# Kernel optimization log

Hardware: AMD Instinct MI355X
Metric: run time of the kernel (lower is better)

Reference implementation:

```python
import jax, jax.numpy as jnp
import numpy as np

B, S, F, D, NH, K, NB = 128, 200, 32, 512, 4, 4, 2
Dh = D // NH
UP = 704  # round(1.3*512) up to multiple of 64
FD = 7    # forecast_days
EPS = 1e-5


def _layernorm(x, w):
    mu = x.mean(-1, keepdims=True)
    var = ((x - mu) ** 2).mean(-1, keepdims=True)
    return (x - mu) / jnp.sqrt(var + EPS) * w


def _forward(x, w_in, b_in, ln1_w, conv_w, conv_b, w_gates, r_gates, b_gates,
             gn_w, ln2_w, ff_up, ff_down, post_ln_w, fc1_w, fc1_b, fc2_w, fc2_b):
    b, s, _ = x.shape
    h = x @ w_in + b_in  # (B,S,D) input projection
    for blk in range(NB):
        xn = _layernorm(h, ln1_w[blk])
        # causal depthwise conv1d (kernel K) + swish, feeds i/f gates
        xp = jnp.pad(xn, ((0, 0), (K - 1, 0), (0, 0)))
        xc = conv_b[blk] + sum(conv_w[blk, k] * xp[:, k:k + s, :] for k in range(K))
        xc = xc * jax.nn.sigmoid(xc)  # swish
        xch = xc.reshape(b, s, NH, Dh)
        xnh = xn.reshape(b, s, NH, Dh)
        # headwise (block-diagonal) gate projections
        ipre = jnp.einsum('bshd,hde->bshe', xch, w_gates[blk, 0])
        fpre = jnp.einsum('bshd,hde->bshe', xch, w_gates[blk, 1])
        zpre = jnp.einsum('bshd,hde->bshe', xnh, w_gates[blk, 2])
        opre = jnp.einsum('bshd,hde->bshe', xnh, w_gates[blk, 3])
        pre = jnp.stack([ipre, fpre, zpre, opre], 0)        # (4,B,S,NH,Dh)
        pre = jnp.transpose(pre, (2, 0, 1, 3, 4))           # (S,4,B,NH,Dh)
        R = r_gates[blk]                                     # (4,NH,Dh,Dh)
        bg = b_gates[blk].reshape(4, NH, Dh)

        def step(carry, g):
            hs, cs, ns, ms = carry  # each (B,NH,Dh)
            rec = jnp.einsum('bhd,ghde->gbhe', hs, R)
            iraw = g[0] + rec[0] + bg[0]
            fraw = g[1] + rec[1] + bg[1]
            zraw = g[2] + rec[2] + bg[2]
            oraw = g[3] + rec[3] + bg[3]
            # stabilized exponential gating (vanilla sLSTM backend)
            logf = ms + jax.nn.log_sigmoid(fraw)
            m_new = jnp.maximum(iraw, logf)
            ig = jnp.exp(iraw - m_new)
            fg = jnp.exp(logf - m_new)
            c_new = fg * cs + ig * jnp.tanh(zraw)
            n_new = fg * ns + ig
            h_new = jax.nn.sigmoid(oraw) * c_new / n_new
            return (h_new, c_new, n_new, m_new), h_new

        z0 = jnp.zeros((b, NH, Dh), x.dtype)
        _, hseq = jax.lax.scan(step, (z0, z0, z0, z0), pre)  # (S,B,NH,Dh)
        # multi-head groupnorm (per head, over Dh)
        mu = hseq.mean(-1, keepdims=True)
        var = ((hseq - mu) ** 2).mean(-1, keepdims=True)
        y = (hseq - mu) / jnp.sqrt(var + EPS) * gn_w[blk].reshape(NH, Dh)
        y = jnp.transpose(y, (1, 0, 2, 3)).reshape(b, s, D)
        h = h + y  # residual
        # gated GeLU feedforward with residual
        xn2 = _layernorm(h, ln2_w[blk])
        u = xn2 @ ff_up[blk]                                 # (B,S,2*UP)
        gate, up = jnp.split(u, 2, -1)
        h = h + (jax.nn.gelu(gate) * up) @ ff_down[blk]
    h = _layernorm(h, post_ln_w)  # post-blocks norm
    last = h[:, -1, :]
    out = jax.nn.relu(last @ fc1_w + fc1_b) @ fc2_w + fc2_b  # (B,FD)
    return out


def setup_inputs() -> dict:
    key = jax.random.key(0)
    ks = jax.random.split(key, 12)

    def rn(k, shape, s=0.02):
        return jax.random.normal(k, shape, jnp.float32) * s

    return {
        'x': jax.random.normal(ks[0], (B, S, F), jnp.float32),
        'w_in': rn(ks[1], (F, D), 0.1),
        'b_in': jnp.zeros((D,), jnp.float32),
        'ln1_w': jnp.ones((NB, D), jnp.float32),
        'conv_w': rn(ks[2], (NB, K, D), 0.1),
        'conv_b': jnp.zeros((NB, D), jnp.float32),
        'w_gates': rn(ks[3], (NB, 4, NH, Dh, Dh), 0.05),
        'r_gates': rn(ks[4], (NB, 4, NH, Dh, Dh), 0.05),
        'b_gates': rn(ks[5], (NB, 4, D), 0.1),
        'gn_w': jnp.ones((NB, D), jnp.float32),
        'ln2_w': jnp.ones((NB, D), jnp.float32),
        'ff_up': rn(ks[6], (NB, D, 2 * UP), 0.05),
        'ff_down': rn(ks[7], (NB, UP, D), 0.05),
        'post_ln_w': jnp.ones((D,), jnp.float32),
        'fc1_w': rn(ks[8], (D, D // 2), 0.05),
        'fc1_b': jnp.zeros((D // 2,), jnp.float32),
        'fc2_w': rn(ks[9], (D // 2, FD), 0.05),
        'fc2_b': jnp.zeros((FD,), jnp.float32),
    }


def reference(x, w_in, b_in, ln1_w, conv_w, conv_b, w_gates, r_gates, b_gates,
              gn_w, ln2_w, ff_up, ff_down, post_ln_w, fc1_w, fc1_b, fc2_w, fc2_b):
    return _forward(x, w_in, b_in, ln1_w, conv_w, conv_b, w_gates, r_gates, b_gates,
                    gn_w, ln2_w, ff_up, ff_down, post_ln_w, fc1_w, fc1_b, fc2_w, fc2_b)
```

## Files before the change

### kernel.cpp

```cpp
#include <hip/hip_runtime.h>

#define B_  128
#define S_  200
#define F_  32
#define D_  512
#define NH_ 4
#define DH_ 128
#define KK_ 4
#define NB_ 2
#define UP_ 704
#define FD_ 7
#define M_  (B_*S_)

typedef unsigned short u16;
typedef _Float16 f16;
typedef __attribute__((ext_vector_type(8))) _Float16 f16x8;
typedef __attribute__((ext_vector_type(8))) short  s16x8;
typedef __attribute__((ext_vector_type(4))) float  f32x4;

__device__ __forceinline__ u16 f2bf(float f){
  unsigned x = __builtin_bit_cast(unsigned, f);
  return (u16)((x + 0x7fffu + ((x>>16)&1u)) >> 16);
}
__device__ __forceinline__ float bf2f(u16 u){
  return __builtin_bit_cast(float, (unsigned)u << 16);
}
__device__ __forceinline__ f32x4 mfma16(s16x8 a, s16x8 b, f32x4 c){
  return __builtin_amdgcn_mfma_f32_16x16x32_bf16(a, b, c, 0, 0, 0);
}
__device__ __forceinline__ f32x4 mfma16h(f16x8 a, f16x8 b, f32x4 c){
  return __builtin_amdgcn_mfma_f32_16x16x32_f16(a, b, c, 0, 0, 0);
}
__device__ __forceinline__ float frcp(float x){ return __builtin_amdgcn_rcpf(x); }
__device__ __forceinline__ float tanh_fast(float z){
  const float u = __expf(-2.f*fabsf(z));
  const float t = (1.f-u)*frcp(1.f+u);
  return copysignf(t, z);
}
__device__ __forceinline__ float logsig_fast(float f){
  const float t = __expf(-fabsf(f));
  return fminf(f, 0.f) - __logf(1.f + t);
}
__device__ __forceinline__ float sigmoid_fast(float x){
  return frcp(1.f + __expf(-x));
}
__device__ __forceinline__ void bar_lgkm(){
  __builtin_amdgcn_sched_barrier(0);
  asm volatile("s_waitcnt lgkmcnt(0)" ::: "memory");
  __builtin_amdgcn_s_barrier();
  __builtin_amdgcn_sched_barrier(0);
}
template<int CTRL>
__device__ __forceinline__ float dpp_add(float v){
  int x = __builtin_amdgcn_update_dpp(0, __builtin_bit_cast(int, v), CTRL, 0xf, 0xf, false);
  return v + __builtin_bit_cast(float, x);
}
__device__ __forceinline__ float wave_sum64(float v){
  v = dpp_add<0x111>(v);
  v = dpp_add<0x112>(v);
  v = dpp_add<0x114>(v);
  v = dpp_add<0x118>(v);
  v = dpp_add<0x142>(v);
  v = dpp_add<0x143>(v);
  return __builtin_bit_cast(float, __builtin_amdgcn_readlane(__builtin_bit_cast(int, v), 63));
}

__global__ void k_cast(const float* __restrict__ in, u16* __restrict__ out, int n){
  int i = blockIdx.x*256 + threadIdx.x;
  if (i < n) out[i] = f2bf(in[i]);
}
__global__ void k_cast_up(const float* __restrict__ in, u16* __restrict__ out, int n){
  int i = blockIdx.x*256 + threadIdx.x;
  if (i >= n) return;
  const int np   = i % (2*UP_);
  const int rest = i / (2*UP_);
  const int k = np >> 7, j = np & 127;
  const int col = (j < 64) ? (k*64 + j) : (UP_ + k*64 + (j - 64));
  out[i] = f2bf(in[(size_t)rest*(2*UP_) + col]);
}
__global__ void k_zero(float* __restrict__ p, int n){
  int i = blockIdx.x*256 + threadIdx.x;
  if (i < n) p[i] = 0.f;
}
__global__ void k_sentinel(float* __restrict__ out, int n){
  int i = blockIdx.x*256 + threadIdx.x;
  if (i < n) out[i] = -12345.0f;
}

__global__ __launch_bounds__(256) void k_inproj(const float* __restrict__ x,
    const float* __restrict__ w, const float* __restrict__ bias, float* __restrict__ h)
{
  __shared__ float xs[8][32];
  const int m0 = blockIdx.x*8, tid = threadIdx.x;
  xs[tid>>5][tid&31] = x[(size_t)(m0 + (tid>>5))*F_ + (tid&31)];
  __syncthreads();
  #pragma unroll
  for (int hf=0; hf<2; ++hf){
    const int e = tid + hf*256;
    float a[8];
    const float bb = bias[e];
    #pragma unroll
    for (int r=0;r<8;r++) a[r]=bb;
    for (int f=0; f<F_; ++f){
      const float wv = w[(size_t)f*D_ + e];
      #pragma unroll
      for (int r=0;r<8;r++) a[r] += xs[r][f]*wv;
    }
    #pragma unroll
    for (int r=0;r<8;r++) h[(size_t)(m0+r)*D_ + e] = a[r];
  }
}

__global__ __launch_bounds__(128) void k_ln(const float* __restrict__ in, const float* __restrict__ w,
      u16* __restrict__ outb)
{
  const int row = blockIdx.x, tid = threadIdx.x;
  const f32x4* rp = (const f32x4*)(in + (size_t)row*D_);
  f32x4 v = rp[tid];
  float s = v[0]+v[1]+v[2]+v[3];
  float q = v[0]*v[0]+v[1]*v[1]+v[2]*v[2]+v[3]*v[3];
  #pragma unroll
  for (int off=32; off; off>>=1){ s += __shfl_down(s,off,64); q += __shfl_down(q,off,64); }
  __shared__ float red[2][2];
  if ((tid&63)==0){ red[tid>>6][0]=s; red[tid>>6][1]=q; }
  __syncthreads();
  const float sum = red[0][0]+red[1][0], sq = red[0][1]+red[1][1];
  const float mu  = sum*(1.f/D_);
  const float var = sq*(1.f/D_) - mu*mu;
  const float inv = rsqrtf(var + 1e-5f);
  f32x4 wv = ((const f32x4*)w)[tid];
  ushort4 ob;
  ob.x=f2bf((v[0]-mu)*inv*wv[0]); ob.y=f2bf((v[1]-mu)*inv*wv[1]);
  ob.z=f2bf((v[2]-mu)*inv*wv[2]); ob.w=f2bf((v[3]-mu)*inv*wv[3]);
  ((ushort4*)(outb + (size_t)row*D_))[tid] = ob;
}

__global__ __launch_bounds__(128) void k_addln(float* __restrict__ h, const u16* __restrict__ y,
      const float* __restrict__ w, u16* __restrict__ outb)
{
  const int row = blockIdx.x, tid = threadIdx.x;
  f32x4 v = ((const f32x4*)(h + (size_t)row*D_))[tid];
  ushort4 yq = ((const ushort4*)(y + (size_t)row*D_))[tid];
  v[0]+=bf2f(yq.x); v[1]+=bf2f(yq.y); v[2]+=bf2f(yq.z); v[3]+=bf2f(yq.w);
  ((f32x4*)(h + (size_t)row*D_))[tid] = v;
  float s = v[0]+v[1]+v[2]+v[3];
  float q = v[0]*v[0]+v[1]*v[1]+v[2]*v[2]+v[3]*v[3];
  #pragma unroll
  for (int off=32; off; off>>=1){ s += __shfl_down(s,off,64); q += __shfl_down(q,off,64); }
  __shared__ float red[2][2];
  if ((tid&63)==0){ red[tid>>6][0]=s; red[tid>>6][1]=q; }
  __syncthreads();
  const float sum = red[0][0]+red[1][0], sq = red[0][1]+red[1][1];
  const float mu  = sum*(1.f/D_);
  const float var = sq*(1.f/D_) - mu*mu;
  const float inv = rsqrtf(var + 1e-5f);
  f32x4 wv = ((const f32x4*)w)[tid];
  ushort4 ob;
  ob.x=f2bf((v[0]-mu)*inv*wv[0]); ob.y=f2bf((v[1]-mu)*inv*wv[1]);
  ob.z=f2bf((v[2]-mu)*inv*wv[2]); ob.w=f2bf((v[3]-mu)*inv*wv[3]);
  ((ushort4*)(outb + (size_t)row*D_))[tid] = ob;
}

__global__ void k_conv(const u16* __restrict__ xnbf, const float* __restrict__ cw,
                       const float* __restrict__ cb, u16* __restrict__ xcc,
                       int s0, int Sc)
{
  const int idx = blockIdx.x*256 + threadIdx.x;
  const int e4 = idx & 127;
  const int sl = (idx >> 7) % Sc;
  const int b  = idx / (128*Sc);
  const int s  = s0 + sl;
  f32x4 acc = ((const f32x4*)cb)[e4];
  #pragma unroll
  for (int k=0;k<KK_;k++){
    const int sp = s - (KK_-1) + k;
    if (sp >= 0){
      f32x4 w4 = ((const f32x4*)cw)[k*128 + e4];
      ushort4 xq = ((const ushort4*)xnbf)[(size_t)(b*S_ + sp)*128 + e4];
      acc[0] += w4[0]*bf2f(xq.x);
      acc[1] += w4[1]*bf2f(xq.y);
      acc[2] += w4[2]*bf2f(xq.z);
      acc[3] += w4[3]*bf2f(xq.w);
    }
  }
  ushort4 o;
  float a;
  a=acc[0]; o.x=f2bf(a*sigmoid_fast(a));
  a=acc[1]; o.y=f2bf(a*sigmoid_fast(a));
  a=acc[2]; o.z=f2bf(a*sigmoid_fast(a));
  a=acc[3]; o.w=f2bf(a*sigmoid_fast(a));
  ((ushort4*)xcc)[idx] = o;
}

__global__ __launch_bounds__(256) void k_gemm_ffn(
    const u16* __restrict__ A, int lda,
    const u16* __restrict__ Bw, int ldb,
    float* __restrict__ C, int ldc,
    int Kdim, int addmode)
{
  __shared__ u16 As[128*40];
  __shared__ u16 Bs[128*40];
  const int tid = threadIdx.x;
  const int m0 = blockIdx.x * 128;
  const int n0 = blockIdx.y * 128;
  const int w = tid >> 6, l = tid & 63;
  const int l16 = l & 15, kg = l >> 4;
  f32x4 acc[2][8];
  #pragma unroll
  for (int i=0;i<2;i++)
    #pragma unroll
    for (int j=0;j<8;j++) acc[i][j] = (f32x4)0.f;
  const int nk = Kdim >> 5;
  for (int kt=0; kt<nk; ++kt){
    const int k0 = kt<<5;
    __syncthreads();
    #pragma unroll
    for (int p=0;p<2;p++){
      const int idx = p*256 + tid;
      const int row = idx>>2, kc = (idx&3)*8;
      s16x8 v = *(const s16x8*)(A + (size_t)(m0+row)*lda + k0 + kc);
      *(s16x8*)&As[row*40 + kc] = v;
    }
    {
      const int kp = tid>>4; const int nn = (tid&15)*8;
      const u16* bp = Bw + (size_t)(k0 + 2*kp)*ldb + n0 + nn;
      s16x8 r0 = *(const s16x8*)bp;
      s16x8 r1 = *(const s16x8*)(bp + ldb);
      #pragma unroll
      for (int j=0;j<8;j++){
        unsigned uu = (unsigned)(u16)r0[j] | ((unsigned)(u16)r1[j]<<16);
        *(unsigned*)&Bs[(nn+j)*40 + 2*kp] = uu;
      }
    }
    __syncthreads();
    s16x8 af[2];
    #pragma unroll
    for (int mf=0;mf<2;mf++)
      af[mf] = *(const s16x8*)&As[(w*32 + mf*16 + l16)*40 + kg*8];
    #pragma unroll
    for (int nf=0;nf<8;nf++){
      s16x8 bfr = *(const s16x8*)&Bs[(nf*16 + l16)*40 + kg*8];
      #pragma unroll
      for (int mf=0;mf<2;mf++)
        acc[mf][nf] = mfma16(af[mf], bfr, acc[mf][nf]);
    }
  }
  #pragma unroll
  for (int mf=0;mf<2;mf++){
    #pragma unroll
    for (int j=0;j<4;j++){
      const int row = m0 + w*32 + mf*16 + kg*4 + j;
      float* cp = C + (size_t)row*ldc + n0 + l16;
      #pragma unroll
      for (int nf=0;nf<8;nf++){
        const float v = acc[mf][nf][j];
        if (addmode) cp[nf*16] += v; else cp[nf*16] = v;
      }
    }
  }
}

__global__ __launch_bounds__(256) void k_gemm_up(
    const u16* __restrict__ A,
    const u16* __restrict__ Bw,
    u16* __restrict__ act)
{
  __shared__ u16 As[128*40];
  __shared__ u16 Bs[128*40];
  const int tid = threadIdx.x;
  const int m0 = blockIdx.x * 128;
  const int n0 = blockIdx.y * 128;
  const int w = tid >> 6, l = tid & 63;
  const int l16 = l & 15, kg = l >> 4;
  f32x4 acc[2][8];
  #pragma unroll
  for (int i=0;i<2;i++)
    #pragma unroll
    for (int j=0;j<8;j++) acc[i][j] = (f32x4)0.f;
  for (int kt=0; kt<16; ++kt){
    const int k0 = kt<<5;
    __syncthreads();
    #pragma unroll
    for (int p=0;p<2;p++){
      const int idx = p*256 + tid;
      const int row = idx>>2, kc = (idx&3)*8;
      s16x8 v = *(const s16x8*)(A + (size_t)(m0+row)*D_ + k0 + kc);
      *(s16x8*)&As[row*40 + kc] = v;
    }
    {
      const int kp = tid>>4; const int nn = (tid&15)*8;
      const u16* bp = Bw + (size_t)(k0 + 2*kp)*(2*UP_) + n0 + nn;
      s16x8 r0 = *(const s16x8*)bp;
      s16x8 r1 = *(const s16x8*)(bp + 2*UP_);
      #pragma unroll
      for (int j=0;j<8;j++){
        unsigned uu = (unsigned)(u16)r0[j] | ((unsigned)(u16)r1[j]<<16);
        *(unsigned*)&Bs[(nn+j)*40 + 2*kp] = uu;
      }
    }
    __syncthreads();
    s16x8 af[2];
    #pragma unroll
    for (int mf=0;mf<2;mf++)
      af[mf] = *(const s16x8*)&As[(w*32 + mf*16 + l16)*40 + kg*8];
    #pragma unroll
    for (int nf=0;nf<8;nf++){
      s16x8 bfr = *(const s16x8*)&Bs[(nf*16 + l16)*40 + kg*8];
      #pragma unroll
      for (int mf=0;mf<2;mf++)
        acc[mf][nf] = mfma16(af[mf], bfr, acc[mf][nf]);
    }
  }
  const int n0h = blockIdx.y * 64;
  #pragma unroll
  for (int mf=0;mf<2;mf++){
    #pragma unroll
    for (int j=0;j<4;j++){
      const int row = m0 + w*32 + mf*16 + kg*4 + j;
      u16* ap = act + (size_t)row*UP_ + n0h + l16;
      #pragma unroll
      for (int nf=0;nf<4;nf++){
        const float gg = acc[mf][nf][j];
        const float uu = acc[mf][nf+4][j];
        const float tt = tanh_fast(0.7978845608028654f*(gg + 0.044715f*gg*gg*gg));
        ap[nf*16] = f2bf(0.5f*gg*(1.f+tt)*uu);
      }
    }
  }
}

__global__ __launch_bounds__(256) void k_gemm_gates(
    const u16* __restrict__ xcc, const u16* __restrict__ xnbf,
    const u16* __restrict__ wg,
    const float* __restrict__ bgates,
    u16* __restrict__ pre, int s0, int Sc)
{
  __shared__ u16 As[128*40];
  __shared__ u16 Bs[128*40];
  const int tid = threadIdx.x;
  const int m0 = blockIdx.x * 128;
  const int gh = blockIdx.y; const int g = gh>>2, hh = gh&3;
  const u16* Bw = wg + (size_t)gh*DH_*DH_;
  const int w = tid >> 6, l = tid & 63;
  const int l16 = l & 15, kg = l >> 4;
  f32x4 acc[2][8];
  #pragma unroll
  for (int i=0;i<2;i++)
    #pragma unroll
    for (int j=0;j<8;j++) acc[i][j] = (f32x4)0.f;
  for (int kt=0; kt<4; ++kt){
    const int k0 = kt<<5;
    __syncthreads();
    #pragma unroll
    for (int p=0;p<2;p++){
      const int idx = p*256 + tid;
      const int row = idx>>2, kc = (idx&3)*8;
      const int m = m0 + row;
      size_t aoff;
      const u16* Abase;
      if (g < 2){ Abase = xcc;  aoff = (size_t)m*D_; }
      else {
        const int b2 = m / Sc, sl2 = m - b2*Sc;
        Abase = xnbf; aoff = (size_t)(b2*S_ + s0 + sl2)*D_;
      }
      s16x8 v = *(const s16x8*)(Abase + aoff + hh*DH_ + k0 + kc);
      *(s16x8*)&As[row*40 + kc] = v;
    }
    {
      const int kp = tid>>4; const int nn = (tid&15)*8;
      const u16* bp = Bw + (size_t)(k0 + 2*kp)*DH_ + nn;
      s16x8 r0 = *(const s16x8*)bp;
      s16x8 r1 = *(const s16x8*)(bp + DH_);
      #pragma unroll
      for (int j=0;j<8;j++){
        unsigned uu = (unsigned)(u16)r0[j] | ((unsigned)(u16)r1[j]<<16);
        *(unsigned*)&Bs[(nn+j)*40 + 2*kp] = uu;
      }
    }
    __syncthreads();
    s16x8 af[2];
    #pragma unroll
    for (int mf=0;mf<2;mf++)
      af[mf] = *(const s16x8*)&As[(w*32 + mf*16 + l16)*40 + kg*8];
    #pragma unroll
    for (int nf=0;nf<8;nf++){
      s16x8 bfr = *(const s16x8*)&Bs[(nf*16 + l16)*40 + kg*8];
      #pragma unroll
      for (int mf=0;mf<2;mf++)
        acc[mf][nf] = mfma16(af[mf], bfr, acc[mf][nf]);
    }
  }
  #pragma unroll
  for (int mf=0;mf<2;mf++){
    #pragma unroll
    for (int j=0;j<4;j++){
      const int m = m0 + w*32 + mf*16 + kg*4 + j;
      const int b2 = m / Sc;
      const int sl2 = m - b2*Sc;
      #pragma unroll
      for (int nf=0;nf<8;nf++){
        const int col = nf*16 + l16;
        const float bias = bgates[g*D_ + hh*128 + col];
        pre[(((size_t)g*Sc + sl2)*B_ + b2)*D_ + hh*128 + col] =
            __builtin_bit_cast(u16, (f16)(acc[mf][nf][j] + bias));
      }
    }
  }
}

__global__ __launch_bounds__(512, 2) void k_scan(
    const u16* __restrict__ pre,
    const float* __restrict__ rg,
    const float* __restrict__ gnw,
    u16* __restrict__ ybuf,
    float* __restrict__ st, int s0, int Sc)
{
  const int t   = threadIdx.x;
  const int hh  = blockIdx.y;
  const int bg0 = blockIdx.x * 2;
  const int w   = t >> 6;
  const int l   = t & 63;
  const int g   = w >> 1;
  const int ch  = w & 1;
  const int la  = l >> 4, lb = l & 15;

  __shared__ __align__(16) char  hA[16*256];
  __shared__ __align__(16) float recl[16*132];
  __shared__ float red[2][2][2];

  f16x8 Rf[4][4];
  {
    const float* rbase = rg + ((size_t)(g*NH_ + hh)*DH_)*DH_ + ch*64;
    #pragma unroll
    for (int ct=0; ct<4; ++ct)
      #pragma unroll
      for (int ks=0; ks<4; ++ks){
        f16x8 f;
        #pragma unroll
        for (int j=0;j<8;j++)
          f[j] = (f16)rbase[(size_t)(ks*32 + la*8 + j)*DH_ + ct*16 + lb];
        Rf[ct][ks] = f;
      }
  }

  const int pb  = t >> 7;
  const int col = t & 127;
  const int wh  = (t >> 6) & 1;
  const bool act = (pb < 2);
  const int pbc = act ? pb : 0;
  const int SCMP = B_*NH_*DH_;
  const int is  = ((bg0+pbc)*NH_ + hh)*128 + col;

  for (int i = t; i < 16*128; i += 512) ((u16*)hA)[i] = 0;
  float hst=0.f, cst=0.f, nst=0.f, mst=0.f;
  if (act){
    hst = st[0*SCMP + is];
    cst = st[1*SCMP + is];
    nst = st[2*SCMP + is];
    mst = st[3*SCMP + is];
    const int slot = col >> 3;
    *(u16*)&hA[pb*256 + (((slot^pb)&15)<<4) + (col&7)*2] = __builtin_bit_cast(u16, (f16)hst);
  }
  const float gws = gnw[hh*128 + col];
  const u16* prebase = pre + (size_t)(bg0+pbc)*D_ + hh*128 + col;
  const size_t gstride = (size_t)Sc*B_*D_;
  const size_t sstride = (size_t)B_*D_;
  u16 pc16[4]={0,0,0,0}, pn16[4]={0,0,0,0};
  if (act){
    #pragma unroll
    for (int g2=0; g2<4; ++g2)
      pc16[g2] = prebase[g2*gstride];
    const int s1c = (Sc > 1) ? 1 : 0;
    #pragma unroll
    for (int g2=0; g2<4; ++g2)
      pn16[g2] = prebase[g2*gstride + (size_t)s1c*sstride];
  }
  __syncthreads();

  for (int sl=0; sl<Sc; ++sl){
    u16 pl16[4]={0,0,0,0};
    if (act){
      const int sn = (sl+2 < Sc) ? sl+2 : Sc-1;
      #pragma unroll
      for (int g2=0; g2<4; ++g2)
        pl16[g2] = prebase[g2*gstride + (size_t)sn*sstride];
    }

    f32x4 accA[4], accB[4];
    #pragma unroll
    for (int ct=0; ct<4; ++ct){ accA[ct] = (f32x4)0.f; accB[ct] = (f32x4)0.f; }
    #pragma unroll
    for (int ks=0; ks<4; ++ks){
      const int slot = ks*4 + la;
      f16x8 af = *(const f16x8*)&hA[lb*256 + (((slot ^ lb)&15)<<4)];
      if (ks < 2){
        #pragma unroll
        for (int ct=0; ct<4; ++ct) accA[ct] = mfma16h(af, Rf[ct][ks], accA[ct]);
      } else {
        #pragma unroll
        for (int ct=0; ct<4; ++ct) accB[ct] = mfma16h(af, Rf[ct][ks], accB[ct]);
      }
    }
    if (la == 0){
      #pragma unroll
      for (int ct=0; ct<4; ++ct){
        recl[(g*4 + 0)*132 + ch*64 + ct*16 + lb] = accA[ct][0] + accB[ct][0];
        recl[(g*4 + 1)*132 + ch*64 + ct*16 + lb] = accA[ct][1] + accB[ct][1];
      }
    }
    bar_lgkm();

    float hv = 0.f;
    if (act){
      const float iraw = (float)__builtin_bit_cast(f16, pc16[0]) + recl[(0*4+pb)*132 + col];
      const float fraw = (float)__builtin_bit_cast(f16, pc16[1]) + recl[(1*4+pb)*132 + col];
      const float zraw = (float)__builtin_bit_cast(f16, pc16[2]) + recl[(2*4+pb)*132 + col];
      const float oraw = (float)__builtin_bit_cast(f16, pc16[3]) + recl[(3*4+pb)*132 + col];
      const float lf   = mst + logsig_fast(fraw);
      const float mn   = fmaxf(iraw, lf);
      const float ig   = __expf(iraw - mn);
      const float fg   = __expf(lf - mn);
      cst = fg*cst + ig*tanh_fast(zraw);
      nst = fg*nst + ig;
      mst = mn;
      hv = sigmoid_fast(oraw) * cst * frcp(nst);
      hst = hv;
      const int slot = col >> 3;
      *(u16*)&hA[pb*256 + (((slot^pb)&15)<<4) + (col&7)*2] = __builtin_bit_cast(u16, (f16)hv);
      const float s1 = wave_sum64(hv);
      const float s2 = wave_sum64(hv*hv);
      if (l == 0){ red[pb][wh][0] = s1; red[pb][wh][1] = s2; }
    }
    bar_lgkm();

    if (act){
      const float sum = red[pb][0][0] + red[pb][1][0];
      const float sq  = red[pb][0][1] + red[pb][1][1];
      const float mu  = sum * (1.f/128.f);
      const float var = sq * (1.f/128.f) - mu*mu;
      const float y   = (hv - mu) * rsqrtf(var + 1e-5f) * gws;
      ybuf[((size_t)(bg0+pb)*S_ + (s0+sl))*D_ + hh*128 + col] = f2bf(y);
      pc16[0]=pn16[0]; pc16[1]=pn16[1]; pc16[2]=pn16[2]; pc16[3]=pn16[3];
      pn16[0]=pl16[0]; pn16[1]=pl16[1]; pn16[2]=pl16[2]; pn16[3]=pl16[3];
    }
  }
  if (act){
    st[0*SCMP + is] = hst;
    st[1*SCMP + is] = cst;
    st[2*SCMP + is] = nst;
    st[3*SCMP + is] = mst;
  }
}

__global__ __launch_bounds__(256) void k_head(const float* __restrict__ h,
     const float* __restrict__ pw, const float* __restrict__ f1w, const float* __restrict__ f1b,
     const float* __restrict__ f2w, const float* __restrict__ f2bias, float* __restrict__ out)
{
  const int b = blockIdx.x, tid = threadIdx.x;
  __shared__ float nrm[512];
  __shared__ float a1[256];
  __shared__ float red[4][2];
  const float* row = h + ((size_t)b*S_ + (S_-1))*D_;
  const float v0 = row[tid], v1 = row[tid+256];
  float s = v0+v1, q = v0*v0+v1*v1;
  #pragma unroll
  for (int off=32; off; off>>=1){ s += __shfl_down(s,off,64); q += __shfl_down(q,off,64); }
  if ((tid&63)==0){ red[tid>>6][0]=s; red[tid>>6][1]=q; }
  __syncthreads();
  const float sum = red[0][0]+red[1][0]+red[2][0]+red[3][0];
  const float sq  = red[0][1]+red[1][1]+red[2][1]+red[3][1];
  const float mu  = sum*(1.f/D_), var = sq*(1.f/D_) - mu*mu;
  const float inv = rsqrtf(var+1e-5f);
  nrm[tid]      = (v0-mu)*inv*pw[tid];
  nrm[tid+256]  = (v1-mu)*inv*pw[tid+256];
  __syncthreads();
  float acc = f1b[tid];
  for (int d=0; d<D_; ++d) acc += nrm[d]*f1w[(size_t)d*256 + tid];
  a1[tid] = fmaxf(acc, 0.f);
  __syncthreads();
  if (tid < FD_){
    float o = f2bias[tid];
    for (int i=0;i<256;++i) o += a1[i]*f2w[(size_t)i*FD_ + tid];
    out[b*FD_ + tid] = o;
  }
}

extern "C" void kernel_launch(void* const* d_in, const int* in_sizes, int n_in,
                              void* d_out, int out_size, void* d_ws, size_t ws_size,
                              hipStream_t stream)
{
  const float* x       = (const float*)d_in[0];
  const float* w_in    = (const float*)d_in[1];
  const float* b_in    = (const float*)d_in[2];
  const float* ln1_w   = (const float*)d_in[3];
  const float* conv_w  = (const float*)d_in[4];
  const float* conv_b  = (const float*)d_in[5];
  const float* w_gates = (const float*)d_in[6];
  const float* r_gates = (const float*)d_in[7];
  const float* b_gates = (const float*)d_in[8];
  const float* gn_w    = (const float*)d_in[9];
  const float* ln2_w   = (const float*)d_in[10];
  const float* ff_up   = (const float*)d_in[11];
  const float* ff_down = (const float*)d_in[12];
  const float* post_ln = (const float*)d_in[13];
  const float* fc1_w   = (const float*)d_in[14];
  const float* fc1_b   = (const float*)d_in[15];
  const float* fc2_w   = (const float*)d_in[16];
  const float* fc2_b   = (const float*)d_in[17];
  float* out = (float*)d_out;

  char* ws = (char*)d_ws;
  const size_t OFF_H     = 0;
  const size_t OFF_XNBF  = 52428800;
  const size_t OFF_WGBF  = 78643200;
  const size_t OFF_UPBF  = 79691776;
  const size_t OFF_DNBF  = 82575360;
  const size_t OFF_STATE = 84017152;
  const size_t OFF_YBUF  = 85065728;
  const size_t OFF_CHUNK = 111280128;

  if (ws_size < OFF_CHUNK + 655360ull){
    k_sentinel<<<4, 256, 0, stream>>>(out, out_size);
    return;
  }
  const size_t CR = ws_size - OFF_CHUNK;
  int Sc = (int)(CR / 655360ull); if (Sc > S_) Sc = S_;
  int Mc = (int)((CR / 1408ull) & ~(size_t)127); if (Mc > M_) Mc = M_;

  float* h     = (float*)(ws + OFF_H);
  u16*   xnbf  = (u16*)  (ws + OFF_XNBF);
  u16*   wgbf  = (u16*)  (ws + OFF_WGBF);
  u16*   upbf  = (u16*)  (ws + OFF_UPBF);
  u16*   dnbf  = (u16*)  (ws + OFF_DNBF);
  float* st    = (float*)(ws + OFF_STATE);
  u16*   ybuf  = (u16*)  (ws + OFF_YBUF);
  u16*   xcc   = (u16*)  (ws + OFF_CHUNK);
  u16*   prec  = (u16*)  (ws + OFF_CHUNK + (size_t)Sc*131072);
  u16*   actc  = (u16*)  (ws + OFF_CHUNK);

  {
    int n1 = NB_*4*NH_*DH_*DH_;  k_cast<<<(n1+255)/256, 256, 0, stream>>>(w_gates, wgbf, n1);
    int n2 = NB_*D_*2*UP_;       k_cast_up<<<(n2+255)/256, 256, 0, stream>>>(ff_up, upbf, n2);
    int n3 = NB_*UP_*D_;         k_cast<<<(n3+255)/256, 256, 0, stream>>>(ff_down, dnbf, n3);
  }

  k_inproj<<<M_/8, 256, 0, stream>>>(x, w_in, b_in, h);

  for (int blk=0; blk<NB_; ++blk){
    k_ln<<<M_, 128, 0, stream>>>(h, ln1_w + blk*D_, xnbf);
    k_zero<<<1024, 256, 0, stream>>>(st, 4*B_*NH_*DH_);
    for (int s0=0; s0<S_; s0+=Sc){
      const int scur = (S_ - s0 < Sc) ? (S_ - s0) : Sc;
      k_conv<<<scur*64, 256, 0, stream>>>(xnbf, conv_w + blk*KK_*D_, conv_b + blk*D_,
                                          xcc, s0, scur);
      dim3 gg((B_*scur)/128, 16);
      k_gemm_gates<<<gg, 256, 0, stream>>>(xcc, xnbf,
          wgbf + (size_t)blk*4*NH_*DH_*DH_, b_gates + (size_t)blk*4*D_, prec, s0, scur);
      dim3 gs(B_/2, NH_);
      k_scan<<<gs, 512, 0, stream>>>(prec, r_gates + (size_t)blk*4*NH_*DH_*DH_,
                                     gn_w + blk*D_, ybuf, st, s0, scur);
    }
    k_addln<<<M_, 128, 0, stream>>>(h, ybuf, ln2_w + blk*D_, xnbf);
    for (int m0c=0; m0c<M_; m0c+=Mc){
      const int mcur = (M_ - m0c < Mc) ? (M_ - m0c) : Mc;
      dim3 g1(mcur/128, (2*UP_)/128);
      k_gemm_up<<<g1, 256, 0, stream>>>(xnbf + (size_t)m0c*D_,
                                        upbf + (size_t)blk*D_*2*UP_, actc);
      dim3 g2(mcur/128, D_/128);
      k_gemm_ffn<<<g2, 256, 0, stream>>>(actc, UP_,
                                         dnbf + (size_t)blk*UP_*D_, D_,
                                         h + (size_t)m0c*D_, D_, UP_, 1);
    }
  }

  k_head<<<B_, 256, 0, stream>>>(h, post_ln, fc1_w, fc1_b, fc2_w, fc2_b, out);
}
```

Baseline: 1.114 ms.

## Restructure sLSTM scan so each wave owns output columns, cutting barriers per step

The recurrent scan kernel is reorganised so each wave computes all four gates for a 16-column slice via MFMA and keeps the results in registers. This removes the shared-memory recl exchange and one of the two block barriers per timestep. The h buffer is double-buffered, and the group-norm statistics are reduced through a shared array and applied one step late, so the normalisation overlaps the next step's matmul. In exchange, only a quarter of lanes (la==0) do the pointwise gate math for two batches each, which adds register pressure and serial work per active lane.

```diff
diff --git a/kernel.cpp b/kernel.cpp
--- a/kernel.cpp
+++ b/kernel.cpp
@@ -55,14 +55,12 @@
   int x = __builtin_amdgcn_update_dpp(0, __builtin_bit_cast(int, v), CTRL, 0xf, 0xf, false);
   return v + __builtin_bit_cast(float, x);
 }
-__device__ __forceinline__ float wave_sum64(float v){
+__device__ __forceinline__ float row16_sum(float v){
   v = dpp_add<0x111>(v);
   v = dpp_add<0x112>(v);
   v = dpp_add<0x114>(v);
   v = dpp_add<0x118>(v);
-  v = dpp_add<0x142>(v);
-  v = dpp_add<0x143>(v);
-  return __builtin_bit_cast(float, __builtin_amdgcn_readlane(__builtin_bit_cast(int, v), 63));
+  return v;
 }
 
 __global__ void k_cast(const float* __restrict__ in, u16* __restrict__ out, int n){
@@ -420,135 +418,158 @@
   const int bg0 = blockIdx.x * 2;
   const int w   = t >> 6;
   const int l   = t & 63;
-  const int g   = w >> 1;
-  const int ch  = w & 1;
   const int la  = l >> 4, lb = l & 15;
 
-  __shared__ __align__(16) char  hA[16*256];
-  __shared__ __align__(16) float recl[16*132];
-  __shared__ float red[2][2][2];
+  __shared__ __align__(16) char  hA[2][16*256];
+  __shared__ __align__(16) float red[2][8][4];
 
   f16x8 Rf[4][4];
-  {
-    const float* rbase = rg + ((size_t)(g*NH_ + hh)*DH_)*DH_ + ch*64;
-    #pragma unroll
-    for (int ct=0; ct<4; ++ct)
-      #pragma unroll
-      for (int ks=0; ks<4; ++ks){
-        f16x8 f;
-        #pragma unroll
-        for (int j=0;j<8;j++)
-          f[j] = (f16)rbase[(size_t)(ks*32 + la*8 + j)*DH_ + ct*16 + lb];
-        Rf[ct][ks] = f;
-      }
-  }
-
-  const int pb  = t >> 7;
-  const int col = t & 127;
-  const int wh  = (t >> 6) & 1;
-  const bool act = (pb < 2);
-  const int pbc = act ? pb : 0;
+  #pragma unroll
+  for (int g=0; g<4; ++g){
+    const float* rbase = rg + ((size_t)(g*NH_ + hh)*DH_)*DH_ + w*16 + lb;
+    #pragma unroll
+    for (int ks=0; ks<4; ++ks){
+      f16x8 f;
+      #pragma unroll
+      for (int j=0;j<8;j++)
+        f[j] = (f16)rbase[(size_t)(ks*32 + la*8 + j)*DH_];
+      Rf[g][ks] = f;
+    }
+  }
+
+  for (int i = t; i < 2*16*128; i += 512) ((u16*)hA)[i] = 0;
+
+  const bool pw = (la == 0);
+  const int col = w*16 + lb;
   const int SCMP = B_*NH_*DH_;
-  const int is  = ((bg0+pbc)*NH_ + hh)*128 + col;
-
-  for (int i = t; i < 16*128; i += 512) ((u16*)hA)[i] = 0;
-  float hst=0.f, cst=0.f, nst=0.f, mst=0.f;
-  if (act){
-    hst = st[0*SCMP + is];
-    cst = st[1*SCMP + is];
-    nst = st[2*SCMP + is];
-    mst = st[3*SCMP + is];
-    const int slot = col >> 3;
-    *(u16*)&hA[pb*256 + (((slot^pb)&15)<<4) + (col&7)*2] = __builtin_bit_cast(u16, (f16)hst);
-  }
-  const float gws = gnw[hh*128 + col];
-  const u16* prebase = pre + (size_t)(bg0+pbc)*D_ + hh*128 + col;
+  float hst[2]={0,0}, cst[2]={0,0}, nst[2]={0,0}, mstv[2]={0,0};
+  float hprev[2]={0,0};
+  float gws = 0.f;
   const size_t gstride = (size_t)Sc*B_*D_;
   const size_t sstride = (size_t)B_*D_;
-  u16 pc16[4]={0,0,0,0}, pn16[4]={0,0,0,0};
-  if (act){
-    #pragma unroll
-    for (int g2=0; g2<4; ++g2)
-      pc16[g2] = prebase[g2*gstride];
+  const u16* preb[2] = {pre, pre};
+  u16 pc16[4][2], pn16[4][2];
+  #pragma unroll
+  for (int g=0; g<4; ++g){ pc16[g][0]=0; pc16[g][1]=0; pn16[g][0]=0; pn16[g][1]=0; }
+  if (pw){
+    gws = gnw[hh*128 + col];
     const int s1c = (Sc > 1) ? 1 : 0;
     #pragma unroll
-    for (int g2=0; g2<4; ++g2)
-      pn16[g2] = prebase[g2*gstride + (size_t)s1c*sstride];
+    for (int b=0;b<2;b++){
+      const int is = ((bg0+b)*NH_ + hh)*128 + col;
+      hst[b]  = st[0*SCMP + is];
+      cst[b]  = st[1*SCMP + is];
+      nst[b]  = st[2*SCMP + is];
+      mstv[b] = st[3*SCMP + is];
+      preb[b] = pre + (size_t)(bg0+b)*D_ + hh*128 + col;
+      const int slot = col >> 3;
+      *(u16*)&hA[0][b*256 + (((slot^b)&15)<<4) + (col&7)*2] = __builtin_bit_cast(u16, (f16)hst[b]);
+      #pragma unroll
+      for (int g=0; g<4; ++g){
+        pc16[g][b] = preb[b][g*gstride];
+        pn16[g][b] = preb[b][g*gstride + (size_t)s1c*sstride];
+      }
+    }
   }
   __syncthreads();
 
   for (int sl=0; sl<Sc; ++sl){
-    u16 pl16[4]={0,0,0,0};
-    if (act){
+    u16 pl16[4][2];
+    #pragma unroll
+    for (int g=0; g<4; ++g){ pl16[g][0]=0; pl16[g][1]=0; }
+    if (pw){
       const int sn = (sl+2 < Sc) ? sl+2 : Sc-1;
       #pragma unroll
-      for (int g2=0; g2<4; ++g2)
-        pl16[g2] = prebase[g2*gstride + (size_t)sn*sstride];
-    }
-
-    f32x4 accA[4], accB[4];
-    #pragma unroll
-    for (int ct=0; ct<4; ++ct){ accA[ct] = (f32x4)0.f; accB[ct] = (f32x4)0.f; }
+      for (int b=0;b<2;b++)
+        #pragma unroll
+        for (int g=0; g<4; ++g)
+          pl16[g][b] = preb[b][g*gstride + (size_t)sn*sstride];
+    }
+
+    f32x4 acc[4];
+    #pragma unroll
+    for (int g=0; g<4; ++g) acc[g] = (f32x4)0.f;
     #pragma unroll
     for (int ks=0; ks<4; ++ks){
       const int slot = ks*4 + la;
-      f16x8 af = *(const f16x8*)&hA[lb*256 + (((slot ^ lb)&15)<<4)];
-      if (ks < 2){
-        #pragma unroll
-        for (int ct=0; ct<4; ++ct) accA[ct] = mfma16h(af, Rf[ct][ks], accA[ct]);
-      } else {
-        #pragma unroll
-        for (int ct=0; ct<4; ++ct) accB[ct] = mfma16h(af, Rf[ct][ks], accB[ct]);
-      }
-    }
-    if (la == 0){
-      #pragma unroll
-      for (int ct=0; ct<4; ++ct){
-        recl[(g*4 + 0)*132 + ch*64 + ct*16 + lb] = accA[ct][0] + accB[ct][0];
-        recl[(g*4 + 1)*132 + ch*64 + ct*16 + lb] = accA[ct][1] + accB[ct][1];
+      f16x8 af = *(const f16x8*)&hA[sl&1][lb*256 + (((slot ^ lb)&15)<<4)];
+      #pragma unroll
+      for (int g=0; g<4; ++g) acc[g] = mfma16h(af, Rf[g][ks], acc[g]);
+    }
+
+    if (pw && sl > 0){
+      const int pb2 = (sl-1)&1;
+      float sum[2]={0,0}, sq[2]={0,0};
+      #pragma unroll
+      for (int w2=0; w2<8; ++w2){
+        f32x4 rv = *(const f32x4*)&red[pb2][w2][0];
+        sum[0]+=rv[0]; sq[0]+=rv[1]; sum[1]+=rv[2]; sq[1]+=rv[3];
+      }
+      #pragma unroll
+      for (int b=0;b<2;b++){
+        const float mu  = sum[b]*(1.f/128.f);
+        const float var = sq[b]*(1.f/128.f) - mu*mu;
+        const float y   = (hprev[b]-mu)*rsqrtf(var+1e-5f)*gws;
+        ybuf[((size_t)(bg0+b)*S_ + (s0+sl-1))*D_ + hh*128 + col] = f2bf(y);
+      }
+    }
+
+    if (pw){
+      float s1b[2], s2b[2];
+      #pragma unroll
+      for (int b=0;b<2;b++){
+        const float iraw = (float)__builtin_bit_cast(f16, pc16[0][b]) + acc[0][b];
+        const float fraw = (float)__builtin_bit_cast(f16, pc16[1][b]) + acc[1][b];
+        const float zraw = (float)__builtin_bit_cast(f16, pc16[2][b]) + acc[2][b];
+        const float oraw = (float)__builtin_bit_cast(f16, pc16[3][b]) + acc[3][b];
+        const float lf   = mstv[b] + logsig_fast(fraw);
+        const float mn   = fmaxf(iraw, lf);
+        const float ig   = __expf(iraw - mn);
+        const float fg   = __expf(lf - mn);
+        cst[b] = fg*cst[b] + ig*tanh_fast(zraw);
+        nst[b] = fg*nst[b] + ig;
+        mstv[b] = mn;
+        const float hv = sigmoid_fast(oraw) * cst[b] * frcp(nst[b]);
+        hst[b] = hv; hprev[b] = hv;
+        const int slot = col >> 3;
+        *(u16*)&hA[(sl+1)&1][b*256 + (((slot^b)&15)<<4) + (col&7)*2] =
+            __builtin_bit_cast(u16, (f16)hv);
+        s1b[b] = row16_sum(hv);
+        s2b[b] = row16_sum(hv*hv);
+      }
+      if (lb == 15){
+        f32x4 rv; rv[0]=s1b[0]; rv[1]=s2b[0]; rv[2]=s1b[1]; rv[3]=s2b[1];
+        *(f32x4*)&red[sl&1][w][0] = rv;
+      }
+      #pragma unroll
+      for (int g=0; g<4; ++g){
+        pc16[g][0]=pn16[g][0]; pc16[g][1]=pn16[g][1];
+        pn16[g][0]=pl16[g][0]; pn16[g][1]=pl16[g][1];
       }
     }
     bar_lgkm();
-
-    float hv = 0.f;
-    if (act){
-      const float iraw = (float)__builtin_bit_cast(f16, pc16[0]) + recl[(0*4+pb)*132 + col];
-      const float fraw = (float)__builtin_bit_cast(f16, pc16[1]) + recl[(1*4+pb)*132 + col];
-      const float zraw = (float)__builtin_bit_cast(f16, pc16[2]) + recl[(2*4+pb)*132 + col];
-      const float oraw = (float)__builtin_bit_cast(f16, pc16[3]) + recl[(3*4+pb)*132 + col];
-      const float lf   = mst + logsig_fast(fraw);
-      const float mn   = fmaxf(iraw, lf);
-      const float ig   = __expf(iraw - mn);
-      const float fg   = __expf(lf - mn);
-      cst = fg*cst + ig*tanh_fast(zraw);
-      nst = fg*nst + ig;
-      mst = mn;
-      hv = sigmoid_fast(oraw) * cst * frcp(nst);
-      hst = hv;
-      const int slot = col >> 3;
-      *(u16*)&hA[pb*256 + (((slot^pb)&15)<<4) + (col&7)*2] = __builtin_bit_cast(u16, (f16)hv);
-      const float s1 = wave_sum64(hv);
-      const float s2 = wave_sum64(hv*hv);
-      if (l == 0){ red[pb][wh][0] = s1; red[pb][wh][1] = s2; }
-    }
-    bar_lgkm();
-
-    if (act){
-      const float sum = red[pb][0][0] + red[pb][1][0];
-      const float sq  = red[pb][0][1] + red[pb][1][1];
-      const float mu  = sum * (1.f/128.f);
-      const float var = sq * (1.f/128.f) - mu*mu;
-      const float y   = (hv - mu) * rsqrtf(var + 1e-5f) * gws;
-      ybuf[((size_t)(bg0+pb)*S_ + (s0+sl))*D_ + hh*128 + col] = f2bf(y);
-      pc16[0]=pn16[0]; pc16[1]=pn16[1]; pc16[2]=pn16[2]; pc16[3]=pn16[3];
-      pn16[0]=pl16[0]; pn16[1]=pl16[1]; pn16[2]=pl16[2]; pn16[3]=pl16[3];
-    }
-  }
-  if (act){
-    st[0*SCMP + is] = hst;
-    st[1*SCMP + is] = cst;
-    st[2*SCMP + is] = nst;
-    st[3*SCMP + is] = mst;
+  }
+
+  if (pw){
+    const int pb2 = (Sc-1)&1;
+    float sum[2]={0,0}, sq[2]={0,0};
+    #pragma unroll
+    for (int w2=0; w2<8; ++w2){
+      f32x4 rv = *(const f32x4*)&red[pb2][w2][0];
+      sum[0]+=rv[0]; sq[0]+=rv[1]; sum[1]+=rv[2]; sq[1]+=rv[3];
+    }
+    #pragma unroll
+    for (int b=0;b<2;b++){
+      const float mu  = sum[b]*(1.f/128.f);
+      const float var = sq[b]*(1.f/128.f) - mu*mu;
+      const float y   = (hprev[b]-mu)*rsqrtf(var+1e-5f)*gws;
+      ybuf[((size_t)(bg0+b)*S_ + (s0+Sc-1))*D_ + hh*128 + col] = f2bf(y);
+      const int is = ((bg0+b)*NH_ + hh)*128 + col;
+      st[0*SCMP + is] = hst[b];
+      st[1*SCMP + is] = cst[b];
+      st[2*SCMP + is] = nst[b];
+      st[3*SCMP + is] = mstv[b];
+    }
   }
 }
 
```

Result: slower. 1.243 ms (+11.6%).

## Prepack bf16 weights into k-slab n-major layout for direct vector B loads

Applied to the files above, without the earlier changes.

The weight cast kernels now write bf16 weights in 32-wide K slabs, each stored n-major with k contiguous. The three MFMA GEMMs (down-proj, up-proj, gates) can then fill the B tile in shared memory with plain 16-byte vector copies. This replaces the per-element pack-two-rows-and-scatter transpose in each k-iteration. The cast kernels now read the fp32 source with strided, uncoalesced gathers, but they run once per call on small weights.

```diff
diff --git a/kernel.cpp b/kernel.cpp
--- a/kernel.cpp
+++ b/kernel.cpp
@@ -65,19 +65,6 @@
   return __builtin_bit_cast(float, __builtin_amdgcn_readlane(__builtin_bit_cast(int, v), 63));
 }
 
-__global__ void k_cast(const float* __restrict__ in, u16* __restrict__ out, int n){
-  int i = blockIdx.x*256 + threadIdx.x;
-  if (i < n) out[i] = f2bf(in[i]);
-}
-__global__ void k_cast_up(const float* __restrict__ in, u16* __restrict__ out, int n){
-  int i = blockIdx.x*256 + threadIdx.x;
-  if (i >= n) return;
-  const int np   = i % (2*UP_);
-  const int rest = i / (2*UP_);
-  const int k = np >> 7, j = np & 127;
-  const int col = (j < 64) ? (k*64 + j) : (UP_ + k*64 + (j - 64));
-  out[i] = f2bf(in[(size_t)rest*(2*UP_) + col]);
-}
 __global__ void k_zero(float* __restrict__ p, int n){
   int i = blockIdx.x*256 + threadIdx.x;
   if (i < n) p[i] = 0.f;
@@ -85,6 +72,44 @@
 __global__ void k_sentinel(float* __restrict__ out, int n){
   int i = blockIdx.x*256 + threadIdx.x;
   if (i < n) out[i] = -12345.0f;
+}
+
+__global__ void k_cast_pack_gates(const float* __restrict__ in, u16* __restrict__ out, int n){
+  int i = blockIdx.x*256 + threadIdx.x;
+  if (i >= n) return;
+  const int mat = i >> 14;
+  const int rem = i & 16383;
+  const int slab = rem >> 12;
+  const int r2   = rem & 4095;
+  const int nn   = r2 >> 5;
+  const int kk   = r2 & 31;
+  out[i] = f2bf(in[(size_t)mat*16384 + (size_t)(slab*32 + kk)*DH_ + nn]);
+}
+__global__ void k_cast_pack_up(const float* __restrict__ in, u16* __restrict__ out, int n){
+  int i = blockIdx.x*256 + threadIdx.x;
+  if (i >= n) return;
+  const int per = 512*1408;
+  const int blk = i / per;
+  const int rem = i - blk*per;
+  const int slab = rem / (1408*32);
+  const int r2   = rem - slab*(1408*32);
+  const int nn   = r2 >> 5;
+  const int kk   = r2 & 31;
+  const int j = nn & 127, tt = nn >> 7;
+  const int col = (j < 64) ? (tt*64 + j) : (UP_ + tt*64 + (j - 64));
+  out[i] = f2bf(in[(size_t)(blk*512 + slab*32 + kk)*(2*UP_) + col]);
+}
+__global__ void k_cast_pack_dn(const float* __restrict__ in, u16* __restrict__ out, int n){
+  int i = blockIdx.x*256 + threadIdx.x;
+  if (i >= n) return;
+  const int per = 704*512;
+  const int blk = i / per;
+  const int rem = i - blk*per;
+  const int slab = rem / (512*32);
+  const int r2   = rem - slab*(512*32);
+  const int nn   = r2 >> 5;
+  const int kk   = r2 & 31;
+  out[i] = f2bf(in[(size_t)(blk*704 + slab*32 + kk)*D_ + nn]);
 }
 
 __global__ __launch_bounds__(256) void k_inproj(const float* __restrict__ x,
@@ -221,16 +246,12 @@
       s16x8 v = *(const s16x8*)(A + (size_t)(m0+row)*lda + k0 + kc);
       *(s16x8*)&As[row*40 + kc] = v;
     }
-    {
-      const int kp = tid>>4; const int nn = (tid&15)*8;
-      const u16* bp = Bw + (size_t)(k0 + 2*kp)*ldb + n0 + nn;
-      s16x8 r0 = *(const s16x8*)bp;
-      s16x8 r1 = *(const s16x8*)(bp + ldb);
-      #pragma unroll
-      for (int j=0;j<8;j++){
-        unsigned uu = (unsigned)(u16)r0[j] | ((unsigned)(u16)r1[j]<<16);
-        *(unsigned*)&Bs[(nn+j)*40 + 2*kp] = uu;
-      }
+    #pragma unroll
+    for (int p=0;p<2;p++){
+      const int idx = p*256 + tid;
+      const int nl = idx>>2, ck = (idx&3)*8;
+      s16x8 v = *(const s16x8*)(Bw + (size_t)kt*ldb*32 + (size_t)(n0+nl)*32 + ck);
+      *(s16x8*)&Bs[nl*40 + ck] = v;
     }
     __syncthreads();
     s16x8 af[2];
@@ -287,16 +308,12 @@
       s16x8 v = *(const s16x8*)(A + (size_t)(m0+row)*D_ + k0 + kc);
       *(s16x8*)&As[row*40 + kc] = v;
     }
-    {
-      const int kp = tid>>4; const int nn = (tid&15)*8;
-      const u16* bp = Bw + (size_t)(k0 + 2*kp)*(2*UP_) + n0 + nn;
-      s16x8 r0 = *(const s16x8*)bp;
-      s16x8 r1 = *(const s16x8*)(bp + 2*UP_);
-      #pragma unroll
-      for (int j=0;j<8;j++){
-        unsigned uu = (unsigned)(u16)r0[j] | ((unsigned)(u16)r1[j]<<16);
-        *(unsigned*)&Bs[(nn+j)*40 + 2*kp] = uu;
-      }
+    #pragma unroll
+    for (int p=0;p<2;p++){
+      const int idx = p*256 + tid;
+      const int nl = idx>>2, ck = (idx&3)*8;
+      s16x8 v = *(const s16x8*)(Bw + (size_t)kt*(2*UP_)*32 + (size_t)(n0+nl)*32 + ck);
+      *(s16x8*)&Bs[nl*40 + ck] = v;
     }
     __syncthreads();
     s16x8 af[2];
@@ -366,16 +383,12 @@
       s16x8 v = *(const s16x8*)(Abase + aoff + hh*DH_ + k0 + kc);
       *(s16x8*)&As[row*40 + kc] = v;
     }
-    {
-      const int kp = tid>>4; const int nn = (tid&15)*8;
-      const u16* bp = Bw + (size_t)(k0 + 2*kp)*DH_ + nn;
-      s16x8 r0 = *(const s16x8*)bp;
-      s16x8 r1 = *(const s16x8*)(bp + DH_);
-      #pragma unroll
-      for (int j=0;j<8;j++){
-        unsigned uu = (unsigned)(u16)r0[j] | ((unsigned)(u16)r1[j]<<16);
-        *(unsigned*)&Bs[(nn+j)*40 + 2*kp] = uu;
-      }
+    #pragma unroll
+    for (int p=0;p<2;p++){
+      const int idx = p*256 + tid;
+      const int nl = idx>>2, ck = (idx&3)*8;
+      s16x8 v = *(const s16x8*)(Bw + (size_t)kt*DH_*32 + (size_t)nl*32 + ck);
+      *(s16x8*)&Bs[nl*40 + ck] = v;
     }
     __syncthreads();
     s16x8 af[2];
@@ -639,9 +652,9 @@
   u16*   actc  = (u16*)  (ws + OFF_CHUNK);
 
   {
-    int n1 = NB_*4*NH_*DH_*DH_;  k_cast<<<(n1+255)/256, 256, 0, stream>>>(w_gates, wgbf, n1);
-    int n2 = NB_*D_*2*UP_;       k_cast_up<<<(n2+255)/256, 256, 0, stream>>>(ff_up, upbf, n2);
-    int n3 = NB_*UP_*D_;         k_cast<<<(n3+255)/256, 256, 0, stream>>>(ff_down, dnbf, n3);
+    int n1 = NB_*4*NH_*DH_*DH_;  k_cast_pack_gates<<<(n1+255)/256, 256, 0, stream>>>(w_gates, wgbf, n1);
+    int n2 = NB_*D_*2*UP_;       k_cast_pack_up<<<(n2+255)/256, 256, 0, stream>>>(ff_up, upbf, n2);
+    int n3 = NB_*UP_*D_;         k_cast_pack_dn<<<(n3+255)/256, 256, 0, stream>>>(ff_down, dnbf, n3);
   }
 
   k_inproj<<<M_/8, 256, 0, stream>>>(x, w_in, b_in, h);
```

Result: faster. 979.0 us, median of 2 (-12.1%).
